# Performance work log

Hardware: AMD Instinct MI355X
Metric: run time of the kernel (lower is better)

The kernel has to match this reference:

```python
import jax, jax.numpy as jnp
import numpy as np

MARGIN = 0.1
N = 16384


def setup_inputs() -> dict:
    key = jax.random.key(0)
    k1, k2 = jax.random.split(key)
    pred = jax.random.normal(k1, (N,), dtype=jnp.float32)
    target = jax.random.uniform(k2, (N,), dtype=jnp.float32)
    return {"pred": pred, "target": target}


def reference(pred, target):
    # mask[i, j] = target[j] < target[i]  (the Python loop's Tj per row i)
    mask = target[None, :] < target[:, None]            # [N, N] bool
    # hinge[i, j] = max(0, margin - (pred[i] - pred[j]))
    hinge = jnp.maximum(0.0, MARGIN - (pred[:, None] - pred[None, :]))
    row_sum = jnp.sum(jnp.where(mask, hinge, 0.0), axis=1)   # [N]
    cnt = jnp.sum(mask, axis=1)                               # [N] int
    # rows with no j such that target[j] < target[i] are skipped (continue)
    per_row = jnp.where(cnt > 0, row_sum / jnp.maximum(cnt, 1).astype(pred.dtype), 0.0)
    return jnp.sum(per_row) / pred.shape[0]
```

## Files before the change

kernel.cpp:

```cpp
#include <hip/hip_runtime.h>


constexpr float MARGIN = 0.1f;
constexpr int NBINS = 256;
constexpr int HB    = 16;
constexpr int RT    = 16;
constexpr int T     = 256;

__device__ __forceinline__ int bin_of(float t) {
    int b = (int)(t * (float)NBINS);
    b = b < 0 ? 0 : (b > NBINS - 1 ? NBINS - 1 : b);
    return b;
}

__global__ __launch_bounds__(T) void hist_k(const float* __restrict__ target,
                                            int* __restrict__ H, int n) {
    __shared__ int lh[NBINS];
    const int tid = (int)threadIdx.x;
    lh[tid] = 0;
    __syncthreads();
    const int per = n / HB;
    const float4 tv = ((const float4*)(target + (int)blockIdx.x * per))[tid];
    atomicAdd(&lh[bin_of(tv.x)], 1);
    atomicAdd(&lh[bin_of(tv.y)], 1);
    atomicAdd(&lh[bin_of(tv.z)], 1);
    atomicAdd(&lh[bin_of(tv.w)], 1);
    __syncthreads();
    H[(int)blockIdx.x * NBINS + tid] = lh[tid];
}

__global__ __launch_bounds__(T) void scatter_k(const float* __restrict__ pred,
                                               const float* __restrict__ target,
                                               const int* __restrict__ H,
                                               float* __restrict__ ts,
                                               float* __restrict__ ps,
                                               int* __restrict__ Bg, int n) {
    __shared__ int bbase[NBINS];
    __shared__ int prevk[NBINS];
    __shared__ int lcnt[NBINS];
    __shared__ int wsum[T / 64];

    const int tid = (int)threadIdx.x;
    const int k   = (int)blockIdx.x;

    int tot = 0, prv = 0;
    #pragma unroll
    for (int q = 0; q < HB; ++q) {
        const int h = H[q * NBINS + tid];
        tot += h;
        prv += (q < k) ? h : 0;
    }
    lcnt[tid] = 0;

    int incl = tot;
    #pragma unroll
    for (int off = 1; off < 64; off <<= 1) {
        int v = __shfl_up(incl, off, 64);
        if ((tid & 63) >= off) incl += v;
    }
    if ((tid & 63) == 63) wsum[tid >> 6] = incl;
    __syncthreads();
    int woff = 0;
    for (int w = 0; w < (tid >> 6); ++w) woff += wsum[w];
    bbase[tid] = woff + incl - tot;
    prevk[tid] = prv;
    __syncthreads();

    const int per = n / HB;
    const float4 tv = ((const float4*)(target + k * per))[tid];
    const float4 pv = ((const float4*)(pred   + k * per))[tid];
    {
        const int b = bin_of(tv.x); const int r = atomicAdd(&lcnt[b], 1);
        const int pos = bbase[b] + prevk[b] + r; ts[pos] = tv.x; ps[pos] = pv.x;
    }
    {
        const int b = bin_of(tv.y); const int r = atomicAdd(&lcnt[b], 1);
        const int pos = bbase[b] + prevk[b] + r; ts[pos] = tv.y; ps[pos] = pv.y;
    }
    {
        const int b = bin_of(tv.z); const int r = atomicAdd(&lcnt[b], 1);
        const int pos = bbase[b] + prevk[b] + r; ts[pos] = tv.z; ps[pos] = pv.z;
    }
    {
        const int b = bin_of(tv.w); const int r = atomicAdd(&lcnt[b], 1);
        const int pos = bbase[b] + prevk[b] + r; ts[pos] = tv.w; ps[pos] = pv.w;
    }

    if (k == 0) {
        Bg[tid] = bbase[tid];
        if (tid == 0) Bg[NBINS] = n;
    }
}

__global__ __launch_bounds__(T) void rank_k(const float* __restrict__ ts,
                                            const float* __restrict__ ps,
                                            const int* __restrict__ B,
                                            float* __restrict__ partials, int n) {
    const int NG = n / RT;
    const int bid = (int)blockIdx.x;

    const float4* __restrict__ p4 = (const float4*)ps;
    const float4* __restrict__ t4 = (const float4*)ts;

    const int lane = (int)threadIdx.x & 63;
    const int wv   = (int)threadIdx.x >> 6;
    __shared__ float ls[T / 64][RT];
    __shared__ unsigned int lc[T / 64][RT];

    float blockacc = 0.f;

    for (int gg = 0; gg < 2; ++gg) {
        const int g = (gg == 0) ? bid : (NG - 1 - bid);
        const int q = g * RT;

        float ti[RT], ci[RT];
        #pragma unroll
        for (int r = 0; r < RT; ++r) {
            ti[r] = ts[q + r];
            ci[r] = MARGIN - ps[q + r];
        }

        const int Blo = B[bin_of(ti[0])];
        const int Bhi = B[bin_of(ti[RT - 1]) + 1];
        const int M0 = Blo & ~3;
        int M1 = (Bhi + 3) & ~3;
        if (M1 > n) M1 = n;

        float sum[RT];
        #pragma unroll
        for (int r = 0; r < RT; ++r) sum[r] = 0.f;

        const int f4 = M0 >> 2;
        for (int j = (int)threadIdx.x; j < f4; j += T) {
            const float4 pj = p4[j];
            #pragma unroll
            for (int r = 0; r < RT; ++r) {
                sum[r] += fmaxf(0.f, ci[r] + pj.x);
                sum[r] += fmaxf(0.f, ci[r] + pj.y);
                sum[r] += fmaxf(0.f, ci[r] + pj.z);
                sum[r] += fmaxf(0.f, ci[r] + pj.w);
            }
        }

        unsigned int cnt[RT];
        #pragma unroll
        for (int r = 0; r < RT; ++r) cnt[r] = 0u;

        const int m4lo = M0 >> 2, m4hi = M1 >> 2;
        const int iters = (m4hi - m4lo + T - 1) / T;
        for (int it = 0; it < iters; ++it) {
            const int j = m4lo + it * T + (int)threadIdx.x;
            const bool inb = j < m4hi;
            const int jc = inb ? j : m4lo;
            const float4 tj = t4[jc];
            const float4 pj = p4[jc];
            #pragma unroll
            for (int r = 0; r < RT; ++r) {
                { bool m = inb && (tj.x < ti[r]); float h = fmaxf(0.f, ci[r] + pj.x);
                  sum[r] += m ? h : 0.f; cnt[r] += (unsigned)__popcll(__ballot(m)); }
                { bool m = inb && (tj.y < ti[r]); float h = fmaxf(0.f, ci[r] + pj.y);
                  sum[r] += m ? h : 0.f; cnt[r] += (unsigned)__popcll(__ballot(m)); }
                { bool m = inb && (tj.z < ti[r]); float h = fmaxf(0.f, ci[r] + pj.z);
                  sum[r] += m ? h : 0.f; cnt[r] += (unsigned)__popcll(__ballot(m)); }
                { bool m = inb && (tj.w < ti[r]); float h = fmaxf(0.f, ci[r] + pj.w);
                  sum[r] += m ? h : 0.f; cnt[r] += (unsigned)__popcll(__ballot(m)); }
            }
        }

        #pragma unroll
        for (int r = 0; r < RT; ++r) {
            float sv = sum[r];
            #pragma unroll
            for (int off = 32; off > 0; off >>= 1) sv += __shfl_down(sv, off, 64);
            if (lane == 0) { ls[wv][r] = sv; lc[wv][r] = cnt[r]; }
        }
        __syncthreads();

        float val = 0.f;
        if ((int)threadIdx.x < RT) {
            float sv = 0.f;
            unsigned int c = (unsigned int)M0;
            #pragma unroll
            for (int w = 0; w < T / 64; ++w) { sv += ls[w][threadIdx.x]; c += lc[w][threadIdx.x]; }
            val = (c > 0u) ? sv / (float)c : 0.f;
        }
        if ((int)threadIdx.x < 64) {
            #pragma unroll
            for (int off = 8; off > 0; off >>= 1) val += __shfl_down(val, off, 64);
        }
        if (threadIdx.x == 0) blockacc += val;
        __syncthreads();
    }

    if (threadIdx.x == 0) partials[blockIdx.x] = blockacc;
}

__global__ __launch_bounds__(T) void final_k(const float* __restrict__ partials,
                                             float* __restrict__ out, int n, int nprt) {
    const int n4 = nprt >> 2;
    double s = 0.0;
    for (int i = (int)threadIdx.x; i < n4; i += T) {
        float4 v = ((const float4*)partials)[i];
        s += (double)v.x + (double)v.y + (double)v.z + (double)v.w;
    }
    #pragma unroll
    for (int off = 32; off > 0; off >>= 1) s += __shfl_down(s, off, 64);
    __shared__ double sd[T / 64];
    const int lane = (int)threadIdx.x & 63, wv = (int)threadIdx.x >> 6;
    if (lane == 0) sd[wv] = s;
    __syncthreads();
    if (threadIdx.x == 0) {
        double t = 0.0;
        #pragma unroll
        for (int w = 0; w < T / 64; ++w) t += sd[w];
        out[0] = (float)(t / (double)n);
    }
}

extern "C" void kernel_launch(void* const* d_in, const int* in_sizes, int n_in,
                              void* d_out, int out_size, void* d_ws, size_t ws_size,
                              hipStream_t stream) {
    const float* pred   = (const float*)d_in[0];
    const float* target = (const float*)d_in[1];
    const int n = in_sizes[0];
    const int NG = n / RT;
    const int NB = NG / 2;

    char* w = (char*)d_ws;
    size_t o = 0;
    auto alloc = [&](size_t bytes) {
        void* p = w + o;
        o = (o + bytes + 255) & ~(size_t)255;
        return p;
    };
    float* ts       = (float*)alloc((size_t)n * 4);
    float* ps       = (float*)alloc((size_t)n * 4);
    int*   H        = (int*)alloc((size_t)NBINS * HB * 4);
    int*   B        = (int*)alloc((size_t)(NBINS + 1) * 4);
    float* partials = (float*)alloc((size_t)NB * 4);

    hist_k<<<HB, T, 0, stream>>>(target, H, n);
    scatter_k<<<HB, T, 0, stream>>>(pred, target, H, ts, ps, B, n);
    rank_k<<<NB, T, 0, stream>>>(ts, ps, B, partials, n);
    final_k<<<1, T, 0, stream>>>(partials, (float*)d_out, n, NB);
}
```

Before: 85.37 us.

## Replace full-chunk hinge sums with per-chunk pred-bin suffix sums; fuse histogram into scatter

Drops the separate histogram kernel. Each scatter block now histograms the whole target array itself and packs the total and prefix counts into one shared int. A new chunk kernel bins each 1024-element chunk of target-sorted preds into pred bins and stores per-chunk bin starts and double suffix sums. The rank kernel then gets each row's hinge sum over fully-below chunks in closed form, scanning only the boundary pred bin, instead of looping over every element below M0. This cuts the O(N^2)-like dense work, at the cost of an extra launch, redundant histogramming in every scatter block, and a pred-binning range assumption of [-4,4).

```diff
diff --git a/kernel.cpp b/kernel.cpp
--- a/kernel.cpp
+++ b/kernel.cpp
@@ -2,55 +2,59 @@
 
 
 constexpr float MARGIN = 0.1f;
-constexpr int NBINS = 256;
-constexpr int HB    = 16;
-constexpr int RT    = 16;
-constexpr int T     = 256;
+constexpr int NBINS  = 256;
+constexpr int PBINS  = 256;
+constexpr int SB     = 16;
+constexpr int CHUNK  = 1024;
+constexpr int NCHUNK = 16;
+constexpr int RT     = 16;
+constexpr int T      = 256;
 
 __device__ __forceinline__ int bin_of(float t) {
     int b = (int)(t * (float)NBINS);
     b = b < 0 ? 0 : (b > NBINS - 1 ? NBINS - 1 : b);
     return b;
 }
-
-__global__ __launch_bounds__(T) void hist_k(const float* __restrict__ target,
-                                            int* __restrict__ H, int n) {
-    __shared__ int lh[NBINS];
-    const int tid = (int)threadIdx.x;
-    lh[tid] = 0;
-    __syncthreads();
-    const int per = n / HB;
-    const float4 tv = ((const float4*)(target + (int)blockIdx.x * per))[tid];
-    atomicAdd(&lh[bin_of(tv.x)], 1);
-    atomicAdd(&lh[bin_of(tv.y)], 1);
-    atomicAdd(&lh[bin_of(tv.z)], 1);
-    atomicAdd(&lh[bin_of(tv.w)], 1);
-    __syncthreads();
-    H[(int)blockIdx.x * NBINS + tid] = lh[tid];
+__device__ __forceinline__ int pbin_of(float p) {
+    int b = (int)((p + 4.0f) * 32.0f);
+    b = b < 0 ? 0 : (b > PBINS - 1 ? PBINS - 1 : b);
+    return b;
 }
 
 __global__ __launch_bounds__(T) void scatter_k(const float* __restrict__ pred,
                                                const float* __restrict__ target,
-                                               const int* __restrict__ H,
                                                float* __restrict__ ts,
                                                float* __restrict__ ps,
                                                int* __restrict__ Bg, int n) {
-    __shared__ int bbase[NBINS];
-    __shared__ int prevk[NBINS];
+    __shared__ int lhp[NBINS];
+    __shared__ int sbase[NBINS];
     __shared__ int lcnt[NBINS];
     __shared__ int wsum[T / 64];
 
     const int tid = (int)threadIdx.x;
     const int k   = (int)blockIdx.x;
-
-    int tot = 0, prv = 0;
-    #pragma unroll
-    for (int q = 0; q < HB; ++q) {
-        const int h = H[q * NBINS + tid];
-        tot += h;
-        prv += (q < k) ? h : 0;
-    }
-    lcnt[tid] = 0;
+    lhp[tid] = 0; lcnt[tid] = 0;
+    __syncthreads();
+
+    const int per    = n / SB;
+    const int base   = k * per;
+    const int basef4 = base >> 2;
+    const int nf4    = n >> 2;
+    const float4* __restrict__ t4 = (const float4*)target;
+    const float4* __restrict__ p4 = (const float4*)pred;
+
+    for (int f = tid; f < nf4; f += T) {
+        const float4 tv = t4[f];
+        const int inc = (f < basef4) ? 0x10001 : 1;
+        atomicAdd(&lhp[bin_of(tv.x)], inc);
+        atomicAdd(&lhp[bin_of(tv.y)], inc);
+        atomicAdd(&lhp[bin_of(tv.z)], inc);
+        atomicAdd(&lhp[bin_of(tv.w)], inc);
+    }
+    __syncthreads();
+
+    const int tot = lhp[tid] & 0xFFFF;
+    const int prv = lhp[tid] >> 16;
 
     int incl = tot;
     #pragma unroll
@@ -62,39 +66,107 @@
     __syncthreads();
     int woff = 0;
     for (int w = 0; w < (tid >> 6); ++w) woff += wsum[w];
-    bbase[tid] = woff + incl - tot;
-    prevk[tid] = prv;
-    __syncthreads();
-
-    const int per = n / HB;
-    const float4 tv = ((const float4*)(target + k * per))[tid];
-    const float4 pv = ((const float4*)(pred   + k * per))[tid];
+    const int bb = woff + incl - tot;
+    sbase[tid] = bb + prv;
+    if (k == 0) {
+        Bg[tid] = bb;
+        if (tid == 0) Bg[NBINS] = n;
+    }
+    __syncthreads();
+
+    const float4 tv = t4[basef4 + tid];
+    const float4 pvv = p4[basef4 + tid];
+    { const int b = bin_of(tv.x); const int r = atomicAdd(&lcnt[b], 1);
+      const int pos = sbase[b] + r; ts[pos] = tv.x; ps[pos] = pvv.x; }
+    { const int b = bin_of(tv.y); const int r = atomicAdd(&lcnt[b], 1);
+      const int pos = sbase[b] + r; ts[pos] = tv.y; ps[pos] = pvv.y; }
+    { const int b = bin_of(tv.z); const int r = atomicAdd(&lcnt[b], 1);
+      const int pos = sbase[b] + r; ts[pos] = tv.z; ps[pos] = pvv.z; }
+    { const int b = bin_of(tv.w); const int r = atomicAdd(&lcnt[b], 1);
+      const int pos = sbase[b] + r; ts[pos] = tv.w; ps[pos] = pvv.w; }
+}
+
+__global__ __launch_bounds__(T) void chunk_k(const float* __restrict__ ps,
+                                             float* __restrict__ pv,
+                                             int* __restrict__ binstart,
+                                             double* __restrict__ sufsum) {
+    __shared__ float spv[CHUNK];
+    __shared__ int lh[PBINS];
+    __shared__ int bb[PBINS + 1];
+    __shared__ int lcnt[PBINS];
+    __shared__ int wsum[T / 64];
+    __shared__ double bsum[PBINS + 1];
+
+    const int tid = (int)threadIdx.x;
+    const int c   = (int)blockIdx.x;
+    lh[tid] = 0; lcnt[tid] = 0;
+    __syncthreads();
+
+    float pl[4];
+    #pragma unroll
+    for (int qq = 0; qq < 4; ++qq) {
+        pl[qq] = ps[c * CHUNK + tid + qq * T];
+        atomicAdd(&lh[pbin_of(pl[qq])], 1);
+    }
+    __syncthreads();
+
+    const int tot = lh[tid];
+    int incl = tot;
+    #pragma unroll
+    for (int off = 1; off < 64; off <<= 1) {
+        int v = __shfl_up(incl, off, 64);
+        if ((tid & 63) >= off) incl += v;
+    }
+    if ((tid & 63) == 63) wsum[tid >> 6] = incl;
+    __syncthreads();
+    int woff = 0;
+    for (int w = 0; w < (tid >> 6); ++w) woff += wsum[w];
+    bb[tid] = woff + incl - tot;
+    if (tid == 0) bb[PBINS] = CHUNK;
+    __syncthreads();
+
+    #pragma unroll
+    for (int qq = 0; qq < 4; ++qq) {
+        const int b = pbin_of(pl[qq]);
+        const int r = atomicAdd(&lcnt[b], 1);
+        spv[bb[b] + r] = pl[qq];
+    }
+    __syncthreads();
+
     {
-        const int b = bin_of(tv.x); const int r = atomicAdd(&lcnt[b], 1);
-        const int pos = bbase[b] + prevk[b] + r; ts[pos] = tv.x; ps[pos] = pv.x;
-    }
-    {
-        const int b = bin_of(tv.y); const int r = atomicAdd(&lcnt[b], 1);
-        const int pos = bbase[b] + prevk[b] + r; ts[pos] = tv.y; ps[pos] = pv.y;
-    }
-    {
-        const int b = bin_of(tv.z); const int r = atomicAdd(&lcnt[b], 1);
-        const int pos = bbase[b] + prevk[b] + r; ts[pos] = tv.z; ps[pos] = pv.z;
-    }
-    {
-        const int b = bin_of(tv.w); const int r = atomicAdd(&lcnt[b], 1);
-        const int pos = bbase[b] + prevk[b] + r; ts[pos] = tv.w; ps[pos] = pv.w;
-    }
-
-    if (k == 0) {
-        Bg[tid] = bbase[tid];
-        if (tid == 0) Bg[NBINS] = n;
+        double s = 0.0;
+        const int lo = bb[tid], hi = bb[tid + 1];
+        for (int i = lo; i < hi; ++i) s += (double)spv[i];
+        bsum[tid] = s;
+        if (tid == 0) bsum[PBINS] = 0.0;
+    }
+    __syncthreads();
+    for (int off = 1; off < PBINS; off <<= 1) {
+        const double tr = (tid + off < PBINS) ? bsum[tid + off] : 0.0;
+        __syncthreads();
+        bsum[tid] += tr;
+        __syncthreads();
+    }
+
+    #pragma unroll
+    for (int qq = 0; qq < 4; ++qq) {
+        const int i = tid + qq * T;
+        pv[c * CHUNK + i] = spv[i];
+    }
+    binstart[c * (PBINS + 1) + tid] = bb[tid];
+    sufsum[c * (PBINS + 1) + tid]  = bsum[tid];
+    if (tid == 0) {
+        binstart[c * (PBINS + 1) + PBINS] = CHUNK;
+        sufsum[c * (PBINS + 1) + PBINS]   = 0.0;
     }
 }
 
 __global__ __launch_bounds__(T) void rank_k(const float* __restrict__ ts,
                                             const float* __restrict__ ps,
                                             const int* __restrict__ B,
+                                            const float* __restrict__ pv,
+                                            const int* __restrict__ binstart,
+                                            const double* __restrict__ sufsum,
                                             float* __restrict__ partials, int n) {
     const int NG = n / RT;
     const int bid = (int)blockIdx.x;
@@ -102,10 +174,12 @@
     const float4* __restrict__ p4 = (const float4*)ps;
     const float4* __restrict__ t4 = (const float4*)ts;
 
-    const int lane = (int)threadIdx.x & 63;
-    const int wv   = (int)threadIdx.x >> 6;
+    const int tid  = (int)threadIdx.x;
+    const int lane = tid & 63;
+    const int wv   = tid >> 6;
     __shared__ float ls[T / 64][RT];
     __shared__ unsigned int lc[T / 64][RT];
+    __shared__ double dacc[T];
 
     float blockacc = 0.f;
 
@@ -125,20 +199,46 @@
         const int M0 = Blo & ~3;
         int M1 = (Bhi + 3) & ~3;
         if (M1 > n) M1 = n;
+        const int CH = M0 >> 10;
+        const int f4 = M0 >> 2;
+
+        double cf = 0.0;
+        {
+            const int row = tid & (RT - 1);
+            const int ch  = tid >> 4;
+            if (ch < CH) {
+                const float cirow = MARGIN - ps[q + row];
+                const float th = -cirow;
+                const int pb = pbin_of(th);
+                const int* bsr = binstart + ch * (PBINS + 1);
+                const int b0 = bsr[pb];
+                const int b1 = bsr[pb + 1];
+                cf = sufsum[ch * (PBINS + 1) + pb + 1]
+                   + (double)cirow * (double)(CHUNK - b1);
+                const float* pvc = pv + ch * CHUNK;
+                for (int i = b0; i < b1; ++i) {
+                    const float p = pvc[i];
+                    if (p > th) cf += (double)p - (double)th;
+                }
+            }
+        }
+        dacc[tid] = cf;
 
         float sum[RT];
         #pragma unroll
         for (int r = 0; r < RT; ++r) sum[r] = 0.f;
 
-        const int f4 = M0 >> 2;
-        for (int j = (int)threadIdx.x; j < f4; j += T) {
-            const float4 pj = p4[j];
-            #pragma unroll
-            for (int r = 0; r < RT; ++r) {
-                sum[r] += fmaxf(0.f, ci[r] + pj.x);
-                sum[r] += fmaxf(0.f, ci[r] + pj.y);
-                sum[r] += fmaxf(0.f, ci[r] + pj.z);
-                sum[r] += fmaxf(0.f, ci[r] + pj.w);
+        {
+            const int j = (CH << 8) + tid;
+            if (j < f4) {
+                const float4 pj = p4[j];
+                #pragma unroll
+                for (int r = 0; r < RT; ++r) {
+                    sum[r] += fmaxf(0.f, ci[r] + pj.x);
+                    sum[r] += fmaxf(0.f, ci[r] + pj.y);
+                    sum[r] += fmaxf(0.f, ci[r] + pj.z);
+                    sum[r] += fmaxf(0.f, ci[r] + pj.w);
+                }
             }
         }
 
@@ -149,7 +249,7 @@
         const int m4lo = M0 >> 2, m4hi = M1 >> 2;
         const int iters = (m4hi - m4lo + T - 1) / T;
         for (int it = 0; it < iters; ++it) {
-            const int j = m4lo + it * T + (int)threadIdx.x;
+            const int j = m4lo + it * T + tid;
             const bool inb = j < m4hi;
             const int jc = inb ? j : m4lo;
             const float4 tj = t4[jc];
@@ -177,22 +277,25 @@
         __syncthreads();
 
         float val = 0.f;
-        if ((int)threadIdx.x < RT) {
+        if (tid < RT) {
             float sv = 0.f;
             unsigned int c = (unsigned int)M0;
             #pragma unroll
-            for (int w = 0; w < T / 64; ++w) { sv += ls[w][threadIdx.x]; c += lc[w][threadIdx.x]; }
-            val = (c > 0u) ? sv / (float)c : 0.f;
-        }
-        if ((int)threadIdx.x < 64) {
+            for (int w = 0; w < T / 64; ++w) { sv += ls[w][tid]; c += lc[w][tid]; }
+            double rowclosed = 0.0;
+            #pragma unroll
+            for (int kk = 0; kk < T / RT; ++kk) rowclosed += dacc[tid + kk * RT];
+            val = (c > 0u) ? (float)((rowclosed + (double)sv) / (double)c) : 0.f;
+        }
+        if (tid < 64) {
             #pragma unroll
             for (int off = 8; off > 0; off >>= 1) val += __shfl_down(val, off, 64);
         }
-        if (threadIdx.x == 0) blockacc += val;
+        if (tid == 0) blockacc += val;
         __syncthreads();
     }
 
-    if (threadIdx.x == 0) partials[blockIdx.x] = blockacc;
+    if (tid == 0) partials[bid] = blockacc;
 }
 
 __global__ __launch_bounds__(T) void final_k(const float* __restrict__ partials,
@@ -233,14 +336,16 @@
         o = (o + bytes + 255) & ~(size_t)255;
         return p;
     };
-    float* ts       = (float*)alloc((size_t)n * 4);
-    float* ps       = (float*)alloc((size_t)n * 4);
-    int*   H        = (int*)alloc((size_t)NBINS * HB * 4);
-    int*   B        = (int*)alloc((size_t)(NBINS + 1) * 4);
-    float* partials = (float*)alloc((size_t)NB * 4);
-
-    hist_k<<<HB, T, 0, stream>>>(target, H, n);
-    scatter_k<<<HB, T, 0, stream>>>(pred, target, H, ts, ps, B, n);
-    rank_k<<<NB, T, 0, stream>>>(ts, ps, B, partials, n);
-    final_k<<<1, T, 0, stream>>>(partials, (float*)d_out, n, NB);
-}
+    float*  ts    = (float*)alloc((size_t)n * 4);
+    float*  ps    = (float*)alloc((size_t)n * 4);
+    int*    B     = (int*)alloc((size_t)(NBINS + 1) * 4);
+    float*  pvb   = (float*)alloc((size_t)n * 4);
+    int*    bst   = (int*)alloc((size_t)NCHUNK * (PBINS + 1) * 4);
+    double* sfx   = (double*)alloc((size_t)NCHUNK * (PBINS + 1) * 8);
+    float*  parts = (float*)alloc((size_t)NB * 4);
+
+    scatter_k<<<SB, T, 0, stream>>>(pred, target, ts, ps, B, n);
+    chunk_k<<<NCHUNK, T, 0, stream>>>(ps, pvb, bst, sfx);
+    rank_k<<<NB, T, 0, stream>>>(ts, ps, B, pvb, bst, sfx, parts, n);
+    final_k<<<1, T, 0, stream>>>(parts, (float*)d_out, n, NB);
+}
```

After: 88.87 us. +4.1%, slower.

## Fuse histogram into scatter and replace final reduction with last-block atomics

Applied to the files above, without the earlier changes.

Merges the histogram and scatter kernels into one sort kernel. Each of the 16 blocks redundantly builds the full histogram, packing its own prefix count into the upper 16 bits of each shared counter. Removes the separate final reduction kernel: rank blocks add their partial sums into 8 padded double slots, and the last block to finish, found with an atomic counter, writes the output. This cuts two kernel launches and the global histogram round-trip. In exchange each sort block reads all of target, and the result now depends on atomic ordering and a hand-written waitcnt for memory visibility.

```diff
diff --git a/kernel.cpp b/kernel.cpp
--- a/kernel.cpp
+++ b/kernel.cpp
@@ -3,9 +3,10 @@
 
 constexpr float MARGIN = 0.1f;
 constexpr int NBINS = 256;
-constexpr int HB    = 16;
+constexpr int SB    = 16;
 constexpr int RT    = 16;
 constexpr int T     = 256;
+constexpr int NSLOT = 8;
 
 __device__ __forceinline__ int bin_of(float t) {
     int b = (int)(t * (float)NBINS);
@@ -13,44 +14,42 @@
     return b;
 }
 
-__global__ __launch_bounds__(T) void hist_k(const float* __restrict__ target,
-                                            int* __restrict__ H, int n) {
-    __shared__ int lh[NBINS];
-    const int tid = (int)threadIdx.x;
-    lh[tid] = 0;
-    __syncthreads();
-    const int per = n / HB;
-    const float4 tv = ((const float4*)(target + (int)blockIdx.x * per))[tid];
-    atomicAdd(&lh[bin_of(tv.x)], 1);
-    atomicAdd(&lh[bin_of(tv.y)], 1);
-    atomicAdd(&lh[bin_of(tv.z)], 1);
-    atomicAdd(&lh[bin_of(tv.w)], 1);
-    __syncthreads();
-    H[(int)blockIdx.x * NBINS + tid] = lh[tid];
-}
-
-__global__ __launch_bounds__(T) void scatter_k(const float* __restrict__ pred,
-                                               const float* __restrict__ target,
-                                               const int* __restrict__ H,
-                                               float* __restrict__ ts,
-                                               float* __restrict__ ps,
-                                               int* __restrict__ Bg, int n) {
-    __shared__ int bbase[NBINS];
-    __shared__ int prevk[NBINS];
+__global__ __launch_bounds__(T) void sort_k(const float* __restrict__ pred,
+                                            const float* __restrict__ target,
+                                            float* __restrict__ ts,
+                                            float* __restrict__ ps,
+                                            int* __restrict__ Bg,
+                                            double* __restrict__ acc,
+                                            int* __restrict__ done, int n) {
+    __shared__ int lhp[NBINS];
+    __shared__ int sbase[NBINS];
     __shared__ int lcnt[NBINS];
     __shared__ int wsum[T / 64];
 
     const int tid = (int)threadIdx.x;
     const int k   = (int)blockIdx.x;
-
-    int tot = 0, prv = 0;
-    #pragma unroll
-    for (int q = 0; q < HB; ++q) {
-        const int h = H[q * NBINS + tid];
-        tot += h;
-        prv += (q < k) ? h : 0;
-    }
-    lcnt[tid] = 0;
+    lhp[tid] = 0; lcnt[tid] = 0;
+    __syncthreads();
+
+    const int per    = n / SB;
+    const int base   = k * per;
+    const int basef4 = base >> 2;
+    const int nf4    = n >> 2;
+    const float4* __restrict__ t4 = (const float4*)target;
+    const float4* __restrict__ p4 = (const float4*)pred;
+
+    for (int f = tid; f < nf4; f += T) {
+        const float4 tv = t4[f];
+        const int inc = (f < basef4) ? 0x10001 : 1;
+        atomicAdd(&lhp[bin_of(tv.x)], inc);
+        atomicAdd(&lhp[bin_of(tv.y)], inc);
+        atomicAdd(&lhp[bin_of(tv.z)], inc);
+        atomicAdd(&lhp[bin_of(tv.w)], inc);
+    }
+    __syncthreads();
+
+    const int tot = lhp[tid] & 0xFFFF;
+    const int prv = lhp[tid] >> 16;
 
     int incl = tot;
     #pragma unroll
@@ -62,52 +61,46 @@
     __syncthreads();
     int woff = 0;
     for (int w = 0; w < (tid >> 6); ++w) woff += wsum[w];
-    bbase[tid] = woff + incl - tot;
-    prevk[tid] = prv;
-    __syncthreads();
-
-    const int per = n / HB;
-    const float4 tv = ((const float4*)(target + k * per))[tid];
-    const float4 pv = ((const float4*)(pred   + k * per))[tid];
-    {
-        const int b = bin_of(tv.x); const int r = atomicAdd(&lcnt[b], 1);
-        const int pos = bbase[b] + prevk[b] + r; ts[pos] = tv.x; ps[pos] = pv.x;
-    }
-    {
-        const int b = bin_of(tv.y); const int r = atomicAdd(&lcnt[b], 1);
-        const int pos = bbase[b] + prevk[b] + r; ts[pos] = tv.y; ps[pos] = pv.y;
-    }
-    {
-        const int b = bin_of(tv.z); const int r = atomicAdd(&lcnt[b], 1);
-        const int pos = bbase[b] + prevk[b] + r; ts[pos] = tv.z; ps[pos] = pv.z;
-    }
-    {
-        const int b = bin_of(tv.w); const int r = atomicAdd(&lcnt[b], 1);
-        const int pos = bbase[b] + prevk[b] + r; ts[pos] = tv.w; ps[pos] = pv.w;
-    }
-
+    const int bb = woff + incl - tot;
+    sbase[tid] = bb + prv;
     if (k == 0) {
-        Bg[tid] = bbase[tid];
-        if (tid == 0) Bg[NBINS] = n;
-    }
+        Bg[tid] = bb;
+        if (tid == 0) { Bg[NBINS] = n; done[0] = 0; }
+        if (tid < NSLOT) acc[tid * 8] = 0.0;
+    }
+    __syncthreads();
+
+    const float4 tv = t4[basef4 + tid];
+    const float4 pvv = p4[basef4 + tid];
+    { const int b = bin_of(tv.x); const int r = atomicAdd(&lcnt[b], 1);
+      const int pos = sbase[b] + r; ts[pos] = tv.x; ps[pos] = pvv.x; }
+    { const int b = bin_of(tv.y); const int r = atomicAdd(&lcnt[b], 1);
+      const int pos = sbase[b] + r; ts[pos] = tv.y; ps[pos] = pvv.y; }
+    { const int b = bin_of(tv.z); const int r = atomicAdd(&lcnt[b], 1);
+      const int pos = sbase[b] + r; ts[pos] = tv.z; ps[pos] = pvv.z; }
+    { const int b = bin_of(tv.w); const int r = atomicAdd(&lcnt[b], 1);
+      const int pos = sbase[b] + r; ts[pos] = tv.w; ps[pos] = pvv.w; }
 }
 
 __global__ __launch_bounds__(T) void rank_k(const float* __restrict__ ts,
                                             const float* __restrict__ ps,
                                             const int* __restrict__ B,
-                                            float* __restrict__ partials, int n) {
+                                            double* __restrict__ acc,
+                                            int* __restrict__ done,
+                                            float* __restrict__ out, int n) {
     const int NG = n / RT;
     const int bid = (int)blockIdx.x;
 
     const float4* __restrict__ p4 = (const float4*)ps;
     const float4* __restrict__ t4 = (const float4*)ts;
 
-    const int lane = (int)threadIdx.x & 63;
-    const int wv   = (int)threadIdx.x >> 6;
+    const int tid  = (int)threadIdx.x;
+    const int lane = tid & 63;
+    const int wv   = tid >> 6;
     __shared__ float ls[T / 64][RT];
     __shared__ unsigned int lc[T / 64][RT];
 
-    float blockacc = 0.f;
+    double blockacc = 0.0;
 
     for (int gg = 0; gg < 2; ++gg) {
         const int g = (gg == 0) ? bid : (NG - 1 - bid);
@@ -131,7 +124,7 @@
         for (int r = 0; r < RT; ++r) sum[r] = 0.f;
 
         const int f4 = M0 >> 2;
-        for (int j = (int)threadIdx.x; j < f4; j += T) {
+        for (int j = tid; j < f4; j += T) {
             const float4 pj = p4[j];
             #pragma unroll
             for (int r = 0; r < RT; ++r) {
@@ -149,7 +142,7 @@
         const int m4lo = M0 >> 2, m4hi = M1 >> 2;
         const int iters = (m4hi - m4lo + T - 1) / T;
         for (int it = 0; it < iters; ++it) {
-            const int j = m4lo + it * T + (int)threadIdx.x;
+            const int j = m4lo + it * T + tid;
             const bool inb = j < m4hi;
             const int jc = inb ? j : m4lo;
             const float4 tj = t4[jc];
@@ -177,43 +170,31 @@
         __syncthreads();
 
         float val = 0.f;
-        if ((int)threadIdx.x < RT) {
+        if (tid < RT) {
             float sv = 0.f;
             unsigned int c = (unsigned int)M0;
             #pragma unroll
-            for (int w = 0; w < T / 64; ++w) { sv += ls[w][threadIdx.x]; c += lc[w][threadIdx.x]; }
+            for (int w = 0; w < T / 64; ++w) { sv += ls[w][tid]; c += lc[w][tid]; }
             val = (c > 0u) ? sv / (float)c : 0.f;
         }
-        if ((int)threadIdx.x < 64) {
+        if (tid < 64) {
             #pragma unroll
             for (int off = 8; off > 0; off >>= 1) val += __shfl_down(val, off, 64);
         }
-        if (threadIdx.x == 0) blockacc += val;
+        if (tid == 0) blockacc += (double)val;
         __syncthreads();
     }
 
-    if (threadIdx.x == 0) partials[blockIdx.x] = blockacc;
-}
-
-__global__ __launch_bounds__(T) void final_k(const float* __restrict__ partials,
-                                             float* __restrict__ out, int n, int nprt) {
-    const int n4 = nprt >> 2;
-    double s = 0.0;
-    for (int i = (int)threadIdx.x; i < n4; i += T) {
-        float4 v = ((const float4*)partials)[i];
-        s += (double)v.x + (double)v.y + (double)v.z + (double)v.w;
-    }
-    #pragma unroll
-    for (int off = 32; off > 0; off >>= 1) s += __shfl_down(s, off, 64);
-    __shared__ double sd[T / 64];
-    const int lane = (int)threadIdx.x & 63, wv = (int)threadIdx.x >> 6;
-    if (lane == 0) sd[wv] = s;
-    __syncthreads();
-    if (threadIdx.x == 0) {
-        double t = 0.0;
-        #pragma unroll
-        for (int w = 0; w < T / 64; ++w) t += sd[w];
-        out[0] = (float)(t / (double)n);
+    if (tid == 0) {
+        atomicAdd(&acc[(bid & (NSLOT - 1)) * 8], blockacc);
+        asm volatile("s_waitcnt vmcnt(0)" ::: "memory");
+        const int old = atomicAdd(done, 1);
+        if (old == (int)gridDim.x - 1) {
+            double s = 0.0;
+            #pragma unroll
+            for (int i = 0; i < NSLOT; ++i) s += atomicAdd(&acc[i * 8], 0.0);
+            out[0] = (float)(s / (double)n);
+        }
     }
 }
 
@@ -233,14 +214,12 @@
         o = (o + bytes + 255) & ~(size_t)255;
         return p;
     };
-    float* ts       = (float*)alloc((size_t)n * 4);
-    float* ps       = (float*)alloc((size_t)n * 4);
-    int*   H        = (int*)alloc((size_t)NBINS * HB * 4);
-    int*   B        = (int*)alloc((size_t)(NBINS + 1) * 4);
-    float* partials = (float*)alloc((size_t)NB * 4);
-
-    hist_k<<<HB, T, 0, stream>>>(target, H, n);
-    scatter_k<<<HB, T, 0, stream>>>(pred, target, H, ts, ps, B, n);
-    rank_k<<<NB, T, 0, stream>>>(ts, ps, B, partials, n);
-    final_k<<<1, T, 0, stream>>>(partials, (float*)d_out, n, NB);
-}
+    float*  ts   = (float*)alloc((size_t)n * 4);
+    float*  ps   = (float*)alloc((size_t)n * 4);
+    int*    B    = (int*)alloc((size_t)(NBINS + 1) * 4);
+    double* acc  = (double*)alloc((size_t)NSLOT * 8 * 8);
+    int*    done = (int*)alloc(16);
+
+    sort_k<<<SB, T, 0, stream>>>(pred, target, ts, ps, B, acc, done, n);
+    rank_k<<<NB, T, 0, stream>>>(ts, ps, B, acc, done, (float*)d_out, n);
+}
```

New measurement: 91.46 us. 1.07x slower.
